# Kernel tuning notes

Hardware: AMD Instinct MI355X
Metric: run time of the kernel (lower is better)

## Reference

```python
import jax, jax.numpy as jnp
import numpy as np

EMBED_DIM = 128
NUM_HEADS = 16
D_K = EMBED_DIM // NUM_HEADS  # 8 quantum wires


def setup_inputs() -> dict:
    key = jax.random.key(0)
    k_x, k_theta, k_w = jax.random.split(key, 3)
    x = jax.random.normal(k_x, (2, 2048, EMBED_DIM), dtype=jnp.float32)
    # trainable RX angles, one per wire (shared across q/k/v since the same
    # q_layer is applied three times in the original module)
    theta = jax.random.normal(k_theta, (D_K,), dtype=jnp.float32)
    # combine_heads Linear(embed_dim, embed_dim, bias=False): weight [out, in]
    bound = 1.0 / np.sqrt(EMBED_DIM)
    W_combine = jax.random.uniform(k_w, (EMBED_DIM, EMBED_DIM), dtype=jnp.float32,
                                   minval=-bound, maxval=bound)
    return {"x": x, "theta": theta, "W_combine": W_combine}


def reference(x, theta, W_combine):
    B, S, E = x.shape
    H, dk = NUM_HEADS, D_K
    # Quantum circuit closed form: RX(x_i) encode then RX(theta_i), no
    # entanglement -> <PauliZ_i> = cos(x_i + theta_i), per token per head.
    z = jnp.cos(x.reshape(B, S, H, dk) + theta)          # [B,S,H,dk]
    # q = k = v = z (same _apply_q applied to x three times)
    qh = z.transpose(0, 2, 1, 3)                          # [B,H,S,dk]
    scores = jnp.einsum("bhsd,bhtd->bhst", qh, qh) / jnp.sqrt(jnp.float32(dk))
    attn = jax.nn.softmax(scores, axis=-1)                # [B,H,S,S]
    out = jnp.einsum("bhst,bhtd->bhsd", attn, qh)         # [B,H,S,dk]
    out = out.transpose(0, 2, 1, 3).reshape(B, S, E)      # [B,S,E]
    return out @ W_combine.T
```

## Files before the change

### kernel.cpp

```cpp
#include <hip/hip_runtime.h>

#define SEQ   2048
#define EMB   128
#define NH    16
#define NB    2
#define NBH   (NB * NH)
#define QB    128
#define NQB   (SEQ / QB)
#define SEQ_H 1024
#define K1_THREADS 512

typedef _Float16 half_t;
typedef _Float16 half4  __attribute__((ext_vector_type(4)));
typedef __fp16   fp16x2 __attribute__((ext_vector_type(2)));
typedef float    floatx16 __attribute__((ext_vector_type(16)));

#define SMEM_BYTES 36944
#define ZT_OFF     16384
#define ZT_PITCH   2056

__global__ __launch_bounds__(K1_THREADS, 4)
void qattn_mfma_kernel(const float* __restrict__ x,
                       const float* __restrict__ theta,
                       half_t* __restrict__ pD,
                       float* __restrict__ lbuf)
{
    __shared__ __align__(16) char smem[SMEM_BYTES];

    const int tid = threadIdx.x;
    const int bid = blockIdx.x;
    const int c2  = bid & 1;
    const int qb  = (bid >> 1) & (NQB - 1);
    const int bh  = bid >> 5;
    const int b   = bh >> 4;
    const int h   = bh & (NH - 1);

    float th[8];
#pragma unroll
    for (int d = 0; d < 8; ++d) th[d] = theta[d];

    const float4* x4 = (const float4*)x + (size_t)b * SEQ * (EMB / 4) + h * 2;

    half4* zqk0 = (half4*)smem;
    half4* zqk1 = (half4*)(smem + 8192);

#pragma unroll
    for (int i = 0; i < SEQ_H / K1_THREADS; ++i) {
        const int tl = tid + i * K1_THREADS;
        const int tg = c2 * SEQ_H + tl;
        float4 lo  = x4[(size_t)tg * (EMB / 4)];
        float4 hi4 = x4[(size_t)tg * (EMB / 4) + 1];
        float z0 = __cosf(lo.x  + th[0]);
        float z1 = __cosf(lo.y  + th[1]);
        float z2 = __cosf(lo.z  + th[2]);
        float z3 = __cosf(lo.w  + th[3]);
        float z4 = __cosf(hi4.x + th[4]);
        float z5 = __cosf(hi4.y + th[5]);
        float z6 = __cosf(hi4.z + th[6]);
        float z7 = __cosf(hi4.w + th[7]);
        half4 zl, zh;
        zl[0] = (half_t)z0; zl[1] = (half_t)z1; zl[2] = (half_t)z2; zl[3] = (half_t)z3;
        zh[0] = (half_t)z4; zh[1] = (half_t)z5; zh[2] = (half_t)z6; zh[3] = (half_t)z7;
        zqk0[tl] = zl;
        zqk1[tl] = zh;
#pragma unroll
        for (int d = 0; d < 4; ++d)
            *(half_t*)(smem + ZT_OFF + d * ZT_PITCH + tl * 2) = zl[d];
#pragma unroll
        for (int d = 0; d < 4; ++d)
            *(half_t*)(smem + ZT_OFF + (4 + d) * ZT_PITCH + tl * 2) = zh[d];
        *(half_t*)(smem + ZT_OFF + 8 * ZT_PITCH + tl * 2) = (half_t)1.0f;
        *(half_t*)(smem + ZT_OFF + 9 * ZT_PITCH + tl * 2) = (half_t)0.0f;
    }

    const int lane = tid & 63;
    const int wid  = tid >> 6;
    const int g    = wid & 3;
    const int c    = wid >> 2;
    const int ln   = lane & 31;
    const int hi   = lane >> 5;

    const float C = 0.35355339059327373f * 1.4426950408889634f;
    const int q = qb * QB + g * 32 + ln;
    float4 xq = ((const float4*)x)[(size_t)(b * SEQ + q) * (EMB / 4) + h * 2 + hi];
    half4 qf;
    qf[0] = (half_t)(__cosf(xq.x + th[4 * hi + 0]) * C);
    qf[1] = (half_t)(__cosf(xq.y + th[4 * hi + 1]) * C);
    qf[2] = (half_t)(__cosf(xq.z + th[4 * hi + 2]) * C);
    qf[3] = (half_t)(__cosf(xq.w + th[4 * hi + 3]) * C);

    __syncthreads();

    const half4* kp  = (hi ? zqk1 : zqk0) + ln;
    const int    dcl = (ln < 9) ? ln : 9;
    const half4* vp  = (const half4*)(smem + ZT_OFF + dcl * ZT_PITCH + hi * 8);

    floatx16 acc = {};
    const floatx16 zero16 = {};
    const int tb = c * (SEQ_H / 2);

#pragma unroll 1
    for (int tt = 0; tt < SEQ_H / 2; tt += 32) {
        const int t0 = tb + tt;
        half4 kf = kp[t0];
        floatx16 s = __builtin_amdgcn_mfma_f32_32x32x8f16(kf, qf, zero16, 0, 0, 0);
        float p[16];
#pragma unroll
        for (int r = 0; r < 16; ++r) p[r] = __builtin_amdgcn_exp2f(s[r]);
#pragma unroll
        for (int w = 0; w < 4; ++w) {
            union { half4 h4; fp16x2 f2[2]; } u;
            u.f2[0] = __builtin_amdgcn_cvt_pkrtz(p[4 * w + 0], p[4 * w + 1]);
            u.f2[1] = __builtin_amdgcn_cvt_pkrtz(p[4 * w + 2], p[4 * w + 3]);
            half4 vf = vp[(t0 >> 2) + 2 * w];
            acc = __builtin_amdgcn_mfma_f32_32x32x8f16(u.h4, vf, acc, 0, 0, 0);
        }
    }

    __syncthreads();
    float* red = (float*)smem;
    const int slot = (g * 64 + lane) * 17;
    if (c == 1) {
#pragma unroll
        for (int r = 0; r < 16; ++r) red[slot + r] = acc[r];
    }
    __syncthreads();
    if (c == 0) {
#pragma unroll
        for (int r = 0; r < 16; ++r) acc[r] += red[slot + r];

        const int q0 = qb * QB + g * 32 + 4 * hi;
        if (ln < 8) {
#pragma unroll
            for (int r = 0; r < 16; ++r) {
                const int qq = q0 + (r & 3) + 8 * (r >> 2);
                pD[((size_t)(b * SEQ + qq) * 2 + c2) * EMB + h * 8 + ln] = (half_t)acc[r];
            }
        } else if (ln == 8) {
#pragma unroll
            for (int r = 0; r < 16; ++r) {
                const int qq = q0 + (r & 3) + 8 * (r >> 2);
                lbuf[(size_t)(b * SEQ + qq) * 32 + c2 * 16 + h] = acc[r];
            }
        }
    }
}

#define K2_ROWS    32
#define K2_THREADS 256
#define XW_PITCH   132

__global__ __launch_bounds__(K2_THREADS)
void combine_mfma_kernel(const half_t* pD,
                         const float* __restrict__ lbuf,
                         const float* __restrict__ W,
                         float* out)
{
    __shared__ half_t Ws[128 * XW_PITCH];
    __shared__ half_t Xs[K2_ROWS * XW_PITCH];

    const int tid   = threadIdx.x;
    const int rbase = blockIdx.x * K2_ROWS;

#pragma unroll
    for (int it = 0; it < 16; ++it) {
        const int idx = tid + it * K2_THREADS;
        const int e   = idx >> 5;
        const int k4  = idx & 31;
        float4 w = ((const float4*)W)[idx];
        union { half4 h4; fp16x2 f2[2]; } u;
        u.f2[0] = __builtin_amdgcn_cvt_pkrtz(w.x, w.y);
        u.f2[1] = __builtin_amdgcn_cvt_pkrtz(w.z, w.w);
        *(half4*)&Ws[e * XW_PITCH + 4 * k4] = u.h4;
    }
#pragma unroll
    for (int it = 0; it < 8; ++it) {
        const int idx = tid + it * K2_THREADS;
        const int r   = idx >> 6;
        const int k2  = idx & 63;
        const int row = rbase + r;
        const half_t* p0 = &pD[(size_t)row * 256 + 2 * k2];
        const int hh = k2 >> 2;
        float l  = lbuf[(size_t)row * 32 + hh] + lbuf[(size_t)row * 32 + 16 + hh];
        float rl = __builtin_amdgcn_rcpf(l);
        float v0 = ((float)p0[0] + (float)p0[128]) * rl;
        float v1 = ((float)p0[1] + (float)p0[129]) * rl;
        *(fp16x2*)&Xs[r * XW_PITCH + 2 * k2] = __builtin_amdgcn_cvt_pkrtz(v0, v1);
    }
    __syncthreads();

    const int lane = tid & 63;
    const int wv   = tid >> 6;
    const int ln   = lane & 31;
    const int hi   = lane >> 5;
    const int e0   = wv * 32;

    floatx16 acc = {};
#pragma unroll
    for (int kk = 0; kk < 16; ++kk) {
        half4 a = *(const half4*)&Xs[ln * XW_PITCH + kk * 8 + hi * 4];
        half4 bf = *(const half4*)&Ws[(e0 + ln) * XW_PITCH + kk * 8 + hi * 4];
        acc = __builtin_amdgcn_mfma_f32_32x32x8f16(a, bf, acc, 0, 0, 0);
    }

#pragma unroll
    for (int reg = 0; reg < 16; ++reg) {
        const int r_loc = (reg & 3) + 8 * (reg >> 2) + 4 * hi;
        out[(size_t)(rbase + r_loc) * EMB + e0 + ln] = acc[reg];
    }
}

extern "C" void kernel_launch(void* const* d_in, const int* in_sizes, int n_in,
                              void* d_out, int out_size, void* d_ws, size_t ws_size,
                              hipStream_t stream) {
    const float* x     = (const float*)d_in[0];
    const float* theta = (const float*)d_in[1];
    const float* W     = (const float*)d_in[2];
    float*  out  = (float*)d_out;
    half_t* pD   = (half_t*)d_out;
    float*  lbuf = (float*)d_ws;

    qattn_mfma_kernel<<<NBH * NQB * 2, K1_THREADS, 0, stream>>>(x, theta, pD, lbuf);
    combine_mfma_kernel<<<(NB * SEQ) / K2_ROWS, K2_THREADS, 0, stream>>>(pD, lbuf, W, out);
}
```

Measured before the change: 28.13 us.

## Precompute cos features in separate kernel and drop split-key reduction

Adds a zprep kernel that computes the cosine features once per (batch, head) into row-major and transposed fp16 workspace buffers, so attention blocks no longer recompute them for every query block. The attention kernel now covers the full sequence per block instead of splitting keys across two blocks. It also normalizes by the softmax denominator in-kernel, which removes the lbuf side buffer and simplifies the combine kernel's input stage. The trade-offs are an extra kernel launch, round-trips of the features through global memory, half as many attention blocks, and a doubled per-block key loop and shared-memory footprint.

```diff
diff --git a/kernel.cpp b/kernel.cpp
--- a/kernel.cpp
+++ b/kernel.cpp
@@ -7,7 +7,6 @@
 #define NBH   (NB * NH)
 #define QB    128
 #define NQB   (SEQ / QB)
-#define SEQ_H 1024
 #define K1_THREADS 512
 
 typedef _Float16 half_t;
@@ -15,62 +14,87 @@
 typedef __fp16   fp16x2 __attribute__((ext_vector_type(2)));
 typedef float    floatx16 __attribute__((ext_vector_type(16)));
 
-#define SMEM_BYTES 36944
-#define ZT_OFF     16384
-#define ZT_PITCH   2056
-
-__global__ __launch_bounds__(K1_THREADS, 4)
-void qattn_mfma_kernel(const float* __restrict__ x,
-                       const float* __restrict__ theta,
-                       half_t* __restrict__ pD,
-                       float* __restrict__ lbuf)
+#define ZROW_H4_PER_BH (2 * SEQ)
+#define ZT_H_PER_BH    (8 * SEQ)
+
+#define ZT_OFF     32768
+#define ZT_PITCH   4112
+#define SMEM_BYTES (ZT_OFF + 9 * ZT_PITCH)
+
+__global__ __launch_bounds__(512)
+void zprep_kernel(const float* __restrict__ x, const float* __restrict__ theta,
+                  half_t* __restrict__ zrow, half_t* __restrict__ zT)
+{
+    const int bh = blockIdx.x >> 2;
+    const int t  = ((blockIdx.x & 3) << 9) | threadIdx.x;
+    const int b  = bh >> 4;
+    const int h  = bh & (NH - 1);
+
+    float th[8];
+#pragma unroll
+    for (int d = 0; d < 8; ++d) th[d] = theta[d];
+
+    const float4* xp = (const float4*)x + (size_t)(b * SEQ + t) * (EMB / 4) + h * 2;
+    float4 lo  = xp[0];
+    float4 hi4 = xp[1];
+    half4 zl, zh;
+    zl[0] = (half_t)__cosf(lo.x  + th[0]);
+    zl[1] = (half_t)__cosf(lo.y  + th[1]);
+    zl[2] = (half_t)__cosf(lo.z  + th[2]);
+    zl[3] = (half_t)__cosf(lo.w  + th[3]);
+    zh[0] = (half_t)__cosf(hi4.x + th[4]);
+    zh[1] = (half_t)__cosf(hi4.y + th[5]);
+    zh[2] = (half_t)__cosf(hi4.z + th[6]);
+    zh[3] = (half_t)__cosf(hi4.w + th[7]);
+
+    half4* zr = (half4*)zrow + (size_t)bh * ZROW_H4_PER_BH;
+    zr[t]       = zl;
+    zr[SEQ + t] = zh;
+
+    half_t* zt = zT + (size_t)bh * ZT_H_PER_BH;
+    zt[0 * SEQ + t] = zl[0];
+    zt[1 * SEQ + t] = zl[1];
+    zt[2 * SEQ + t] = zl[2];
+    zt[3 * SEQ + t] = zl[3];
+    zt[4 * SEQ + t] = zh[0];
+    zt[5 * SEQ + t] = zh[1];
+    zt[6 * SEQ + t] = zh[2];
+    zt[7 * SEQ + t] = zh[3];
+}
+
+__global__ __launch_bounds__(K1_THREADS)
+void qattn_mfma_kernel(const half_t* __restrict__ zrow,
+                       const half_t* __restrict__ zT,
+                       half_t* __restrict__ pD)
 {
     __shared__ __align__(16) char smem[SMEM_BYTES];
 
     const int tid = threadIdx.x;
-    const int bid = blockIdx.x;
-    const int c2  = bid & 1;
-    const int qb  = (bid >> 1) & (NQB - 1);
-    const int bh  = bid >> 5;
+    const int qb  = blockIdx.x & (NQB - 1);
+    const int bh  = blockIdx.x >> 4;
     const int b   = bh >> 4;
     const int h   = bh & (NH - 1);
 
-    float th[8];
-#pragma unroll
-    for (int d = 0; d < 8; ++d) th[d] = theta[d];
-
-    const float4* x4 = (const float4*)x + (size_t)b * SEQ * (EMB / 4) + h * 2;
-
-    half4* zqk0 = (half4*)smem;
-    half4* zqk1 = (half4*)(smem + 8192);
-
-#pragma unroll
-    for (int i = 0; i < SEQ_H / K1_THREADS; ++i) {
-        const int tl = tid + i * K1_THREADS;
-        const int tg = c2 * SEQ_H + tl;
-        float4 lo  = x4[(size_t)tg * (EMB / 4)];
-        float4 hi4 = x4[(size_t)tg * (EMB / 4) + 1];
-        float z0 = __cosf(lo.x  + th[0]);
-        float z1 = __cosf(lo.y  + th[1]);
-        float z2 = __cosf(lo.z  + th[2]);
-        float z3 = __cosf(lo.w  + th[3]);
-        float z4 = __cosf(hi4.x + th[4]);
-        float z5 = __cosf(hi4.y + th[5]);
-        float z6 = __cosf(hi4.z + th[6]);
-        float z7 = __cosf(hi4.w + th[7]);
-        half4 zl, zh;
-        zl[0] = (half_t)z0; zl[1] = (half_t)z1; zl[2] = (half_t)z2; zl[3] = (half_t)z3;
-        zh[0] = (half_t)z4; zh[1] = (half_t)z5; zh[2] = (half_t)z6; zh[3] = (half_t)z7;
-        zqk0[tl] = zl;
-        zqk1[tl] = zh;
-#pragma unroll
-        for (int d = 0; d < 4; ++d)
-            *(half_t*)(smem + ZT_OFF + d * ZT_PITCH + tl * 2) = zl[d];
-#pragma unroll
-        for (int d = 0; d < 4; ++d)
-            *(half_t*)(smem + ZT_OFF + (4 + d) * ZT_PITCH + tl * 2) = zh[d];
-        *(half_t*)(smem + ZT_OFF + 8 * ZT_PITCH + tl * 2) = (half_t)1.0f;
-        *(half_t*)(smem + ZT_OFF + 9 * ZT_PITCH + tl * 2) = (half_t)0.0f;
+    half4* zqk = (half4*)smem;
+    const half4* zr = (const half4*)zrow + (size_t)bh * ZROW_H4_PER_BH;
+#pragma unroll
+    for (int i = 0; i < 4; ++i) {
+        const int idx = tid + i * K1_THREADS;
+        *(float4*)&zqk[idx * 2] = *(const float4*)&zr[idx * 2];
+    }
+    const half_t* ztg = zT + (size_t)bh * ZT_H_PER_BH;
+#pragma unroll
+    for (int i = 0; i < 4; ++i) {
+        const int idx = tid + i * K1_THREADS;
+        const int row = idx >> 8;
+        const int cc  = idx & 255;
+        *(float4*)(smem + ZT_OFF + row * ZT_PITCH + cc * 16) =
+            *(const float4*)&ztg[row * SEQ + cc * 8];
+    }
+    {
+        half4 one4;
+        one4[0] = one4[1] = one4[2] = one4[3] = (half_t)1.0f;
+        *(half4*)(smem + ZT_OFF + 8 * ZT_PITCH + tid * 8) = one4;
     }
 
     const int lane = tid & 63;
@@ -82,25 +106,20 @@
 
     const float C = 0.35355339059327373f * 1.4426950408889634f;
     const int q = qb * QB + g * 32 + ln;
-    float4 xq = ((const float4*)x)[(size_t)(b * SEQ + q) * (EMB / 4) + h * 2 + hi];
-    half4 qf;
-    qf[0] = (half_t)(__cosf(xq.x + th[4 * hi + 0]) * C);
-    qf[1] = (half_t)(__cosf(xq.y + th[4 * hi + 1]) * C);
-    qf[2] = (half_t)(__cosf(xq.z + th[4 * hi + 2]) * C);
-    qf[3] = (half_t)(__cosf(xq.w + th[4 * hi + 3]) * C);
-
-    __syncthreads();
-
-    const half4* kp  = (hi ? zqk1 : zqk0) + ln;
-    const int    dcl = (ln < 9) ? ln : 9;
+    half4 qf = zr[hi * SEQ + q];
+    qf *= (half_t)C;
+
+    __syncthreads();
+
+    const half4* kp  = zqk + hi * SEQ + ln;
+    const int    dcl = (ln < 8) ? ln : 8;
     const half4* vp  = (const half4*)(smem + ZT_OFF + dcl * ZT_PITCH + hi * 8);
-
     floatx16 acc = {};
     const floatx16 zero16 = {};
-    const int tb = c * (SEQ_H / 2);
+    const int tb = c * (SEQ / 2);
 
 #pragma unroll 1
-    for (int tt = 0; tt < SEQ_H / 2; tt += 32) {
+    for (int tt = 0; tt < SEQ / 2; tt += 32) {
         const int t0 = tb + tt;
         half4 kf = kp[t0];
         floatx16 s = __builtin_amdgcn_mfma_f32_32x32x8f16(kf, qf, zero16, 0, 0, 0);
@@ -130,17 +149,16 @@
         for (int r = 0; r < 16; ++r) acc[r] += red[slot + r];
 
         const int q0 = qb * QB + g * 32 + 4 * hi;
+#pragma unroll
+        for (int r = 0; r < 16; ++r) {
+            float lsum = __shfl(acc[r], 8 | (lane & 32), 64);
+            acc[r] *= __builtin_amdgcn_rcpf(lsum);
+        }
         if (ln < 8) {
 #pragma unroll
             for (int r = 0; r < 16; ++r) {
                 const int qq = q0 + (r & 3) + 8 * (r >> 2);
-                pD[((size_t)(b * SEQ + qq) * 2 + c2) * EMB + h * 8 + ln] = (half_t)acc[r];
-            }
-        } else if (ln == 8) {
-#pragma unroll
-            for (int r = 0; r < 16; ++r) {
-                const int qq = q0 + (r & 3) + 8 * (r >> 2);
-                lbuf[(size_t)(b * SEQ + qq) * 32 + c2 * 16 + h] = acc[r];
+                pD[(size_t)(b * SEQ + qq) * 256 + h * 8 + ln] = (half_t)acc[r];
             }
         }
     }
@@ -152,7 +170,6 @@
 
 __global__ __launch_bounds__(K2_THREADS)
 void combine_mfma_kernel(const half_t* pD,
-                         const float* __restrict__ lbuf,
                          const float* __restrict__ W,
                          float* out)
 {
@@ -174,18 +191,12 @@
         *(half4*)&Ws[e * XW_PITCH + 4 * k4] = u.h4;
     }
 #pragma unroll
-    for (int it = 0; it < 8; ++it) {
+    for (int it = 0; it < 4; ++it) {
         const int idx = tid + it * K2_THREADS;
-        const int r   = idx >> 6;
-        const int k2  = idx & 63;
-        const int row = rbase + r;
-        const half_t* p0 = &pD[(size_t)row * 256 + 2 * k2];
-        const int hh = k2 >> 2;
-        float l  = lbuf[(size_t)row * 32 + hh] + lbuf[(size_t)row * 32 + 16 + hh];
-        float rl = __builtin_amdgcn_rcpf(l);
-        float v0 = ((float)p0[0] + (float)p0[128]) * rl;
-        float v1 = ((float)p0[1] + (float)p0[129]) * rl;
-        *(fp16x2*)&Xs[r * XW_PITCH + 2 * k2] = __builtin_amdgcn_cvt_pkrtz(v0, v1);
+        const int r   = idx >> 5;
+        const int cc  = idx & 31;
+        *(half4*)&Xs[r * XW_PITCH + cc * 4] =
+            *(const half4*)&pD[(size_t)(rbase + r) * 256 + cc * 4];
     }
     __syncthreads();
 
@@ -198,7 +209,7 @@
     floatx16 acc = {};
 #pragma unroll
     for (int kk = 0; kk < 16; ++kk) {
-        half4 a = *(const half4*)&Xs[ln * XW_PITCH + kk * 8 + hi * 4];
+        half4 a  = *(const half4*)&Xs[ln * XW_PITCH + kk * 8 + hi * 4];
         half4 bf = *(const half4*)&Ws[(e0 + ln) * XW_PITCH + kk * 8 + hi * 4];
         acc = __builtin_amdgcn_mfma_f32_32x32x8f16(a, bf, acc, 0, 0, 0);
     }
@@ -218,8 +229,10 @@
     const float* W     = (const float*)d_in[2];
     float*  out  = (float*)d_out;
     half_t* pD   = (half_t*)d_out;
-    float*  lbuf = (float*)d_ws;
-
-    qattn_mfma_kernel<<<NBH * NQB * 2, K1_THREADS, 0, stream>>>(x, theta, pD, lbuf);
-    combine_mfma_kernel<<<(NB * SEQ) / K2_ROWS, K2_THREADS, 0, stream>>>(pD, lbuf, W, out);
-}
+    half_t* zrow = (half_t*)d_ws;
+    half_t* zT   = (half_t*)d_ws + (size_t)NBH * ZT_H_PER_BH;
+
+    zprep_kernel<<<NBH * 4, 512, 0, stream>>>(x, theta, zrow, zT);
+    qattn_mfma_kernel<<<NBH * NQB, K1_THREADS, 0, stream>>>(zrow, zT, pD);
+    combine_mfma_kernel<<<(NB * SEQ) / K2_ROWS, K2_THREADS, 0, stream>>>(pD, W, out);
+}
```

New measurement: 30.52 us. 8.5% more time.
